# Performance work log

Hardware: AMD Instinct MI355X
Metric: run time of the kernel (lower is better)

## Reference

```python
import jax, jax.numpy as jnp
import numpy as np
from jax import lax

DIM = 192
PATCH = 8


def conv1x1(x, w):
    # x: [b,c,h,w], w: [o,c] (1x1 conv, no bias)
    return jnp.einsum('bchw,oc->bohw', x, w)


def dwconv(x, w, b, pad):
    # depthwise conv, w: [C,1,kh,kw], groups = C
    y = lax.conv_general_dilated(
        x, w, window_strides=(1, 1), padding=((pad, pad), (pad, pad)),
        dimension_numbers=('NCHW', 'OIHW', 'NCHW'),
        feature_group_count=x.shape[1])
    return y + b[None, :, None, None]


def to_patches(x, p):
    b, c, h, w = x.shape
    ph = (-h) % p
    pw = (-w) % p
    x = jnp.pad(x, ((0, 0), (0, 0), (0, ph), (0, pw)))
    H, W = h + ph, w + pw
    x = x.reshape(b, c, H // p, p, W // p, p)
    return x.transpose(0, 1, 2, 4, 3, 5)  # b c nh nw p p


def from_patches(x, h, w):
    b, c, nh, nw, p, _ = x.shape
    x = x.transpose(0, 1, 2, 4, 3, 5).reshape(b, c, nh * p, nw * p)
    return x[:, :, :h, :w]


def setup_inputs() -> dict:
    key = jax.random.key(0)
    ks = jax.random.split(key, 8)
    b, c, h, w = 4, DIM, 256, 256
    x = jax.random.normal(ks[0], (b, c, h, w), jnp.float32)
    wq = jax.random.normal(ks[1], (c, c), jnp.float32) * 0.02
    w_qdw = jax.random.normal(ks[2], (c, 1, 3, 3), jnp.float32) * 0.1
    b_qdw = jnp.zeros((c,), jnp.float32)
    wkv = jax.random.normal(ks[3], (2 * c, c), jnp.float32) * 0.02
    w_kvdw = jax.random.normal(ks[4], (2 * c, 1, 7, 7), jnp.float32) * 0.05
    b_kvdw = jnp.zeros((2 * c,), jnp.float32)
    ln_w = jnp.ones((c,), jnp.float32)
    ln_b = jnp.zeros((c,), jnp.float32)
    w_proj = jax.random.normal(ks[5], (c, c), jnp.float32) * 0.02
    b_proj = jnp.zeros((c,), jnp.float32)
    return {'x': x, 'wq': wq, 'w_qdw': w_qdw, 'b_qdw': b_qdw,
            'wkv': wkv, 'w_kvdw': w_kvdw, 'b_kvdw': b_kvdw,
            'ln_w': ln_w, 'ln_b': ln_b, 'w_proj': w_proj, 'b_proj': b_proj}


def reference(x, wq, w_qdw, b_qdw, wkv, w_kvdw, b_kvdw, ln_w, ln_b, w_proj, b_proj):
    b, c, h, w = x.shape
    p = PATCH
    q = dwconv(conv1x1(x, wq), w_qdw, b_qdw, pad=1)
    kv = dwconv(conv1x1(x, wkv), w_kvdw, b_kvdw, pad=3)
    k, v = kv[:, :c], kv[:, c:]
    qp = to_patches(q, p).astype(jnp.float32)
    kp = to_patches(k, p).astype(jnp.float32)
    out = jnp.fft.irfft2(jnp.fft.rfft2(qp) * jnp.fft.rfft2(kp), s=(p, p))
    out = from_patches(out, h, w)
    # WithBias LayerNorm over channel dim (channels-last LN in original)
    mu = out.mean(axis=1, keepdims=True)
    var = out.var(axis=1, keepdims=True)
    out = (out - mu) / jnp.sqrt(var + 1e-5)
    out = out * ln_w[None, :, None, None] + ln_b[None, :, None, None]
    out = out * v
    out = conv1x1(out, w_proj) + b_proj[None, :, None, None]
    return out
```

## Files before the change

kernel.cpp:

```cpp
#include <hip/hip_runtime.h>
#include <hip/hip_bf16.h>

#define HW 65536
#define IMG 256
static constexpr int CDIM = 192;

typedef __attribute__((ext_vector_type(8))) short short8;
typedef __attribute__((ext_vector_type(4))) float f32x4;

static __device__ __forceinline__ float b2f(unsigned short u) {
    union { unsigned u; float f; } t; t.u = ((unsigned)u) << 16; return t.f;
}
static __device__ __forceinline__ unsigned short f2bu(float f) {
    __hip_bfloat16 h = __float2bfloat16(f);
    return *reinterpret_cast<unsigned short*>(&h);
}

__global__ void pack_weights(const float* __restrict__ wq,
                             const float* __restrict__ wkv,
                             const float* __restrict__ wp,
                             __hip_bfloat16* __restrict__ Wqkv,
                             __hip_bfloat16* __restrict__ Wp) {
    int i = blockIdx.x * 256 + threadIdx.x;
    if (i < 36864) Wqkv[i] = __float2bfloat16(wq[i]);
    else if (i < 110592) Wqkv[i] = __float2bfloat16(wkv[i - 36864]);
    else if (i < 147456) Wp[i - 110592] = __float2bfloat16(wp[i - 110592]);
}

__global__ void transpose_cvt(const float* __restrict__ x,
                              __hip_bfloat16* __restrict__ xT) {
    __shared__ float tile[32][33];
    const int p0 = blockIdx.x * 32, c0 = blockIdx.y * 32;
    const int tx = threadIdx.x & 31, ty = threadIdx.x >> 5;
#pragma unroll
    for (int r = 0; r < 4; r++)
        tile[ty + r * 8][tx] = x[(size_t)(c0 + ty + r * 8) * HW + p0 + tx];
    __syncthreads();
#pragma unroll
    for (int r = 0; r < 4; r++)
        xT[(size_t)(p0 + ty + r * 8) * 192 + c0 + tx] =
            __float2bfloat16(tile[tx][ty + r * 8]);
}

__global__ void gemm_bf16(const __hip_bfloat16* __restrict__ A,
                          const __hip_bfloat16* __restrict__ Bt,
                          __hip_bfloat16* __restrict__ Y) {
    __shared__ short Bs[128][200];
    const int tid = threadIdx.x;
    const int wid = tid >> 6, lane = tid & 63;
    const int mBase = blockIdx.x * 64, nBase = blockIdx.y * 128;

#pragma unroll
    for (int l = 0; l < 12; l++) {
        int ch = tid + l * 256;
        int row = ch / 24, cc = ch % 24;
        short8 v = *(const short8*)(Bt + (size_t)(nBase + row) * 192 + cc * 8);
        *(short8*)&Bs[row][cc * 8] = v;
    }
    __syncthreads();

    const int lr = lane & 15, lg = lane >> 4;
    const __hip_bfloat16* Ab = A + (size_t)(mBase + wid * 16 + lr) * 192 + lg * 8;
    f32x4 acc[8];
#pragma unroll
    for (int f = 0; f < 8; f++) acc[f] = (f32x4){0.f, 0.f, 0.f, 0.f};

#pragma unroll
    for (int ks = 0; ks < 6; ks++) {
        short8 af = *(const short8*)(Ab + ks * 32);
#pragma unroll
        for (int f = 0; f < 8; f++) {
            short8 bfr = *(const short8*)&Bs[f * 16 + lr][ks * 32 + lg * 8];
            acc[f] = __builtin_amdgcn_mfma_f32_16x16x32_bf16(af, bfr, acc[f], 0, 0, 0);
        }
    }

    const int mrow = mBase + wid * 16 + lg * 4;
#pragma unroll
    for (int f = 0; f < 8; f++) {
        int n = nBase + f * 16 + lr;
#pragma unroll
        for (int r = 0; r < 4; r++)
            Y[(size_t)(mrow + r) * HW + n] = __float2bfloat16(acc[f][r]);
    }
}

__global__ __launch_bounds__(256) void dwconv7_v3(
    const __hip_bfloat16* __restrict__ in,
    const float* __restrict__ wdw,
    const float* __restrict__ bias,
    __hip_bfloat16* __restrict__ out) {
    __shared__ float tile[70][136];
    const int c = blockIdx.y;
    const int x0 = (blockIdx.x & 1) * 128;
    const int y0 = (blockIdx.x >> 1) * 64;
    const __hip_bfloat16* src = in + (size_t)c * HW;

    float w49[49];
#pragma unroll
    for (int i = 0; i < 49; i++) w49[i] = wdw[c * 49 + i];
    const float bval = bias[c];

#pragma unroll
    for (int l = 0; l < 5; l++) {
        int idx = threadIdx.x + l * 256;
        if (idx < 70 * 17) {
            int r = idx / 17, cs = idx - r * 17;
            int gy = y0 + r - 3;
            int gxb = x0 + cs * 8 - 3;
            if ((unsigned)gy < IMG && gxb >= 0 && gxb + 8 <= IMG) {
                short8 v = *(const short8*)(src + gy * IMG + gxb);
                f32x4 lo, hi;
#pragma unroll
                for (int e = 0; e < 4; e++) {
                    lo[e] = b2f((unsigned short)v[e]);
                    hi[e] = b2f((unsigned short)v[4 + e]);
                }
                *(f32x4*)&tile[r][cs * 8] = lo;
                *(f32x4*)&tile[r][cs * 8 + 4] = hi;
            } else {
#pragma unroll
                for (int e = 0; e < 8; e++) {
                    int gx = gxb + e;
                    float val = 0.f;
                    if ((unsigned)gy < IMG && (unsigned)gx < IMG)
                        val = b2f(*(const unsigned short*)(src + gy * IMG + gx));
                    tile[r][cs * 8 + e] = val;
                }
            }
        }
    }
    __syncthreads();

    const int tx4 = (threadIdx.x & 31) * 4;
    const int gy8 = (threadIdx.x >> 5) * 8;
    float acc[8][4];
#pragma unroll
    for (int j = 0; j < 8; j++)
#pragma unroll
        for (int xx = 0; xx < 4; xx++) acc[j][xx] = bval;

#pragma unroll
    for (int rr = 0; rr < 14; rr++) {
        f32x4 wa = *(const f32x4*)&tile[gy8 + rr][tx4];
        f32x4 wb = *(const f32x4*)&tile[gy8 + rr][tx4 + 4];
        f32x4 wc = *(const f32x4*)&tile[gy8 + rr][tx4 + 8];
        float win[12] = {wa[0], wa[1], wa[2], wa[3],
                         wb[0], wb[1], wb[2], wb[3],
                         wc[0], wc[1], wc[2], wc[3]};
#pragma unroll
        for (int j = 0; j < 8; j++) {
            const int ky = rr - j;
            if (ky >= 0 && ky < 7) {
#pragma unroll
                for (int kx = 0; kx < 7; kx++)
#pragma unroll
                    for (int xx = 0; xx < 4; xx++)
                        acc[j][xx] += win[xx + kx] * w49[ky * 7 + kx];
            }
        }
    }

    __hip_bfloat16* dst = out + (size_t)c * HW + (size_t)(y0 + gy8) * IMG + x0 + tx4;
#pragma unroll
    for (int j = 0; j < 8; j++) {
        union { unsigned short h[4]; unsigned long long u; } ob;
#pragma unroll
        for (int xx = 0; xx < 4; xx++) ob.h[xx] = f2bu(acc[j][xx]);
        *(unsigned long long*)(dst + (size_t)j * IMG) = ob.u;
    }
}

__global__ __launch_bounds__(256) void circ_qfused(
    const __hip_bfloat16* __restrict__ q0,
    const __hip_bfloat16* __restrict__ kbuf,
    const float* __restrict__ w_qdw, const float* __restrict__ b_qdw,
    __hip_bfloat16* __restrict__ sout) {
    __shared__ float qs[10][264];
    __shared__ float qP[32][68];
    __shared__ float kP[32][68];
    const int c = blockIdx.y, ph = blockIdx.x;
    const int y0 = ph * 8;
    const __hip_bfloat16* qsrc = q0 + (size_t)c * HW;
    const __hip_bfloat16* ksrc = kbuf + (size_t)c * HW;

    for (int idx = threadIdx.x; idx < 10 * 258; idx += 256) {
        int ly = idx / 258, lx = idx - ly * 258;
        int gy = y0 + ly - 1, gx = lx - 1;
        float v = 0.f;
        if ((unsigned)gy < IMG && (unsigned)gx < IMG)
            v = b2f(*(const unsigned short*)(qsrc + gy * IMG + gx));
        qs[ly][lx] = v;
    }
    {
        const int x = threadIdx.x;
#pragma unroll
        for (int a = 0; a < 8; a++) {
            float v = b2f(*(const unsigned short*)(ksrc + (y0 + a) * IMG + x));
            kP[x >> 3][a * 8 + (x & 7)] = v;
        }
    }
    __syncthreads();

    {
        const int x = threadIdx.x;
        float w9[9];
#pragma unroll
        for (int i = 0; i < 9; i++) w9[i] = w_qdw[c * 9 + i];
        float accq[8];
#pragma unroll
        for (int j = 0; j < 8; j++) accq[j] = b_qdw[c];
#pragma unroll
        for (int kx = 0; kx < 3; kx++)
#pragma unroll
            for (int yy = 0; yy < 10; yy++) {
                float vv = qs[yy][x + kx];
#pragma unroll
                for (int j = 0; j < 8; j++) {
                    int ky = yy - j;
                    if (ky >= 0 && ky < 3) accq[j] += vv * w9[ky * 3 + kx];
                }
            }
#pragma unroll
        for (int j = 0; j < 8; j++) qP[x >> 3][j * 8 + (x & 7)] = accq[j];
    }
    __syncthreads();

    const int i = threadIdx.x >> 5, pw = threadIdx.x & 31;
    float qv[8][8];
#pragma unroll
    for (int a = 0; a < 8; a++) {
        f32x4 u0 = *(const f32x4*)&qP[pw][a * 8];
        f32x4 u1 = *(const f32x4*)&qP[pw][a * 8 + 4];
        qv[a][0] = u0[0]; qv[a][1] = u0[1]; qv[a][2] = u0[2]; qv[a][3] = u0[3];
        qv[a][4] = u1[0]; qv[a][5] = u1[1]; qv[a][6] = u1[2]; qv[a][7] = u1[3];
    }
    float acc[8];
#pragma unroll
    for (int j = 0; j < 8; j++) acc[j] = 0.f;
#pragma unroll
    for (int a = 0; a < 8; a++) {
        const int r = (i - a + 8) & 7;
        f32x4 k0v = *(const f32x4*)&kP[pw][r * 8];
        f32x4 k1v = *(const f32x4*)&kP[pw][r * 8 + 4];
        float kr[8] = {k0v[0], k0v[1], k0v[2], k0v[3],
                       k1v[0], k1v[1], k1v[2], k1v[3]};
#pragma unroll
        for (int b = 0; b < 8; b++)
#pragma unroll
            for (int j = 0; j < 8; j++)
                acc[j] += qv[a][b] * kr[(j - b + 8) & 7];
    }
    union { unsigned short h[8]; short8 s8; } ob;
#pragma unroll
    for (int j = 0; j < 8; j++) ob.h[j] = f2bu(acc[j]);
    *(short8*)(sout + (size_t)c * HW + (size_t)(y0 + i) * IMG + pw * 8) = ob.s8;
}

__global__ __launch_bounds__(256, 2) void gemm_proj_ln(
    const __hip_bfloat16* __restrict__ Wp,
    const __hip_bfloat16* __restrict__ s,
    const __hip_bfloat16* __restrict__ v,
    const float* __restrict__ ln_w, const float* __restrict__ ln_b,
    const float* __restrict__ bias,
    float* __restrict__ Y) {
    __shared__ short Bs[128][200];
    __shared__ float red[2][2][128];
    __shared__ float muA[128], rsA[128];
    const int tid = threadIdx.x;
    const int p0 = blockIdx.x * 128;
    const int px = tid & 127, h = tid >> 7;
    const unsigned short* sp = (const unsigned short*)s;

    float sum = 0.f, sq = 0.f;
#pragma unroll 4
    for (int l = 0; l < 48; l++) {
        int c = h * 96 + l * 2;
        unsigned short ua = sp[(size_t)c * HW + p0 + px];
        unsigned short ub = sp[(size_t)(c + 1) * HW + p0 + px];
        float a = b2f(ua), b = b2f(ub);
        sum += a + b;
        sq += a * a + b * b;
        *(unsigned*)&Bs[px][c] = (unsigned)ua | ((unsigned)ub << 16);
    }
    red[h][0][px] = sum;
    red[h][1][px] = sq;
    __syncthreads();
    if (tid < 128) {
        float sm = red[0][0][tid] + red[1][0][tid];
        float sQ = red[0][1][tid] + red[1][1][tid];
        float mu = sm * (1.f / 192.f);
        float var = sQ * (1.f / 192.f) - mu * mu;
        muA[tid] = mu;
        rsA[tid] = rsqrtf(var + 1e-5f);
    }
    __syncthreads();

    const float mu = muA[px], rs = rsA[px];
#pragma unroll 4
    for (int l = 0; l < 48; l++) {
        int c = h * 96 + l * 2;
        unsigned pr = *(unsigned*)&Bs[px][c];
        float a = b2f((unsigned short)pr);
        float b = b2f((unsigned short)(pr >> 16));
        float va = b2f(*(const unsigned short*)(v + (size_t)c * HW + p0 + px));
        float vb = b2f(*(const unsigned short*)(v + (size_t)(c + 1) * HW + p0 + px));
        a = ((a - mu) * rs * ln_w[c] + ln_b[c]) * va;
        b = ((b - mu) * rs * ln_w[c + 1] + ln_b[c + 1]) * vb;
        *(unsigned*)&Bs[px][c] = (unsigned)f2bu(a) | ((unsigned)f2bu(b) << 16);
    }
    __syncthreads();

    const int wid = tid >> 6, lane = tid & 63;
    const int lr = lane & 15, lg = lane >> 4;
    f32x4 acc[3][8];
#pragma unroll
    for (int mf = 0; mf < 3; mf++)
#pragma unroll
        for (int f = 0; f < 8; f++) acc[mf][f] = (f32x4){0.f, 0.f, 0.f, 0.f};

#pragma unroll
    for (int ks = 0; ks < 6; ks++) {
        short8 bfr[8];
#pragma unroll
        for (int f = 0; f < 8; f++)
            bfr[f] = *(const short8*)&Bs[f * 16 + lr][ks * 32 + lg * 8];
#pragma unroll
        for (int mf = 0; mf < 3; mf++) {
            int mrow = wid * 48 + mf * 16 + lr;
            short8 af = *(const short8*)(Wp + (size_t)mrow * 192 + ks * 32 + lg * 8);
#pragma unroll
            for (int f = 0; f < 8; f++)
                acc[mf][f] = __builtin_amdgcn_mfma_f32_16x16x32_bf16(af, bfr[f], acc[mf][f], 0, 0, 0);
        }
    }

#pragma unroll
    for (int mf = 0; mf < 3; mf++) {
        int m0 = wid * 48 + mf * 16 + lg * 4;
#pragma unroll
        for (int f = 0; f < 8; f++) {
            int n = p0 + f * 16 + lr;
#pragma unroll
            for (int r = 0; r < 4; r++)
                Y[(size_t)(m0 + r) * HW + n] = acc[mf][f][r] + bias[m0 + r];
        }
    }
}

extern "C" void kernel_launch(void* const* d_in, const int* in_sizes, int n_in,
                              void* d_out, int out_size, void* d_ws, size_t ws_size,
                              hipStream_t stream) {
    const float* x      = (const float*)d_in[0];
    const float* wq     = (const float*)d_in[1];
    const float* w_qdw  = (const float*)d_in[2];
    const float* b_qdw  = (const float*)d_in[3];
    const float* wkv    = (const float*)d_in[4];
    const float* w_kvdw = (const float*)d_in[5];
    const float* b_kvdw = (const float*)d_in[6];
    const float* ln_w   = (const float*)d_in[7];
    const float* ln_b   = (const float*)d_in[8];
    const float* w_proj = (const float*)d_in[9];
    const float* b_proj = (const float*)d_in[10];
    float* out = (float*)d_out;
    char* ws = (char*)d_ws;

    __hip_bfloat16* qkv0  = (__hip_bfloat16*)(ws + 0);
    __hip_bfloat16* kvbuf = (__hip_bfloat16*)(ws + 75497472);
    __hip_bfloat16* sbuf  = (__hip_bfloat16*)(ws + 125829120);
    __hip_bfloat16* xT    = (__hip_bfloat16*)(ws + 150994944);
    __hip_bfloat16* Wqkv  = (__hip_bfloat16*)(ws + 176160768);
    __hip_bfloat16* Wp    = Wqkv + 110592;

    pack_weights<<<576, 256, 0, stream>>>(wq, wkv, w_proj, Wqkv, Wp);

    for (int b = 0; b < 4; b++) {
        const float* xb = x + (size_t)b * CDIM * HW;
        transpose_cvt<<<dim3(HW / 32, 6), 256, 0, stream>>>(xb, xT);
        gemm_bf16<<<dim3(9, HW / 128), 256, 0, stream>>>(Wqkv, xT, qkv0);
        dwconv7_v3<<<dim3(8, 384), 256, 0, stream>>>(qkv0 + (size_t)192 * HW,
                                                     w_kvdw, b_kvdw, kvbuf);
        circ_qfused<<<dim3(32, 192), 256, 0, stream>>>(qkv0, kvbuf,
                                                       w_qdw, b_qdw, sbuf);
        gemm_proj_ln<<<HW / 128, 256, 0, stream>>>(Wp, sbuf,
                                                   kvbuf + (size_t)192 * HW,
                                                   ln_w, ln_b, b_proj,
                                                   out + (size_t)b * CDIM * HW);
    }
}
```

Measured before the change: 758.2 us.

## Batch all four images into single kernel launches via blockIdx.z

Adds a batch dimension through blockIdx.z to every kernel and, when the workspace is large enough, launches each stage once over all four images instead of looping per image. This removes per-launch overhead and small-grid tails across 20 launches. In exchange it needs roughly 600 MB of workspace, and the intermediates no longer stay resident in cache between stages. A fallback keeps the per-image loop when the workspace is too small.

```diff
diff --git a/kernel.cpp b/kernel.cpp
--- a/kernel.cpp
+++ b/kernel.cpp
@@ -7,6 +7,13 @@
 
 typedef __attribute__((ext_vector_type(8))) short short8;
 typedef __attribute__((ext_vector_type(4))) float f32x4;
+
+static constexpr size_t BS_X    = (size_t)CDIM * HW;
+static constexpr size_t BS_XT   = (size_t)HW * 192;
+static constexpr size_t BS_QKV  = (size_t)576 * HW;
+static constexpr size_t BS_KV   = (size_t)384 * HW;
+static constexpr size_t BS_S    = (size_t)192 * HW;
+static constexpr size_t BS_OUT  = (size_t)192 * HW;
 
 static __device__ __forceinline__ float b2f(unsigned short u) {
     union { unsigned u; float f; } t; t.u = ((unsigned)u) << 16; return t.f;
@@ -30,6 +37,8 @@
 __global__ void transpose_cvt(const float* __restrict__ x,
                               __hip_bfloat16* __restrict__ xT) {
     __shared__ float tile[32][33];
+    x  += (size_t)blockIdx.z * BS_X;
+    xT += (size_t)blockIdx.z * BS_XT;
     const int p0 = blockIdx.x * 32, c0 = blockIdx.y * 32;
     const int tx = threadIdx.x & 31, ty = threadIdx.x >> 5;
 #pragma unroll
@@ -46,6 +55,8 @@
                           const __hip_bfloat16* __restrict__ Bt,
                           __hip_bfloat16* __restrict__ Y) {
     __shared__ short Bs[128][200];
+    Bt += (size_t)blockIdx.z * BS_XT;
+    Y  += (size_t)blockIdx.z * BS_QKV;
     const int tid = threadIdx.x;
     const int wid = tid >> 6, lane = tid & 63;
     const int mBase = blockIdx.x * 64, nBase = blockIdx.y * 128;
@@ -91,6 +102,8 @@
     const float* __restrict__ bias,
     __hip_bfloat16* __restrict__ out) {
     __shared__ float tile[70][136];
+    in  += (size_t)blockIdx.z * BS_QKV;
+    out += (size_t)blockIdx.z * BS_KV;
     const int c = blockIdx.y;
     const int x0 = (blockIdx.x & 1) * 128;
     const int y0 = (blockIdx.x >> 1) * 64;
@@ -179,6 +192,9 @@
     __shared__ float qs[10][264];
     __shared__ float qP[32][68];
     __shared__ float kP[32][68];
+    q0   += (size_t)blockIdx.z * BS_QKV;
+    kbuf += (size_t)blockIdx.z * BS_KV;
+    sout += (size_t)blockIdx.z * BS_S;
     const int c = blockIdx.y, ph = blockIdx.x;
     const int y0 = ph * 8;
     const __hip_bfloat16* qsrc = q0 + (size_t)c * HW;
@@ -267,6 +283,9 @@
     __shared__ short Bs[128][200];
     __shared__ float red[2][2][128];
     __shared__ float muA[128], rsA[128];
+    s += (size_t)blockIdx.z * BS_S;
+    v += (size_t)blockIdx.z * BS_KV;
+    Y += (size_t)blockIdx.z * BS_OUT;
     const int tid = threadIdx.x;
     const int p0 = blockIdx.x * 128;
     const int px = tid & 127, h = tid >> 7;
@@ -365,26 +384,46 @@
     float* out = (float*)d_out;
     char* ws = (char*)d_ws;
 
-    __hip_bfloat16* qkv0  = (__hip_bfloat16*)(ws + 0);
-    __hip_bfloat16* kvbuf = (__hip_bfloat16*)(ws + 75497472);
-    __hip_bfloat16* sbuf  = (__hip_bfloat16*)(ws + 125829120);
-    __hip_bfloat16* xT    = (__hip_bfloat16*)(ws + 150994944);
-    __hip_bfloat16* Wqkv  = (__hip_bfloat16*)(ws + 176160768);
-    __hip_bfloat16* Wp    = Wqkv + 110592;
-
-    pack_weights<<<576, 256, 0, stream>>>(wq, wkv, w_proj, Wqkv, Wp);
-
-    for (int b = 0; b < 4; b++) {
-        const float* xb = x + (size_t)b * CDIM * HW;
-        transpose_cvt<<<dim3(HW / 32, 6), 256, 0, stream>>>(xb, xT);
-        gemm_bf16<<<dim3(9, HW / 128), 256, 0, stream>>>(Wqkv, xT, qkv0);
-        dwconv7_v3<<<dim3(8, 384), 256, 0, stream>>>(qkv0 + (size_t)192 * HW,
-                                                     w_kvdw, b_kvdw, kvbuf);
-        circ_qfused<<<dim3(32, 192), 256, 0, stream>>>(qkv0, kvbuf,
-                                                       w_qdw, b_qdw, sbuf);
-        gemm_proj_ln<<<HW / 128, 256, 0, stream>>>(Wp, sbuf,
-                                                   kvbuf + (size_t)192 * HW,
-                                                   ln_w, ln_b, b_proj,
-                                                   out + (size_t)b * CDIM * HW);
-    }
-}
+    const size_t BATCHED_NEED = 604200960ull;
+    const bool batched = (ws_size >= BATCHED_NEED);
+
+    if (batched) {
+        __hip_bfloat16* qkv0  = (__hip_bfloat16*)(ws + 0);
+        __hip_bfloat16* kvbuf = (__hip_bfloat16*)(ws + 301989888ull);
+        __hip_bfloat16* xT    = (__hip_bfloat16*)(ws + 503316480ull);
+        __hip_bfloat16* sbuf  = xT;
+        __hip_bfloat16* Wqkv  = (__hip_bfloat16*)(ws + 603979776ull);
+        __hip_bfloat16* Wp    = Wqkv + 110592;
+
+        pack_weights<<<576, 256, 0, stream>>>(wq, wkv, w_proj, Wqkv, Wp);
+        transpose_cvt<<<dim3(HW / 32, 6, 4), 256, 0, stream>>>(x, xT);
+        gemm_bf16<<<dim3(9, HW / 128, 4), 256, 0, stream>>>(Wqkv, xT, qkv0);
+        dwconv7_v3<<<dim3(8, 384, 4), 256, 0, stream>>>(qkv0 + (size_t)192 * HW,
+                                                        w_kvdw, b_kvdw, kvbuf);
+        circ_qfused<<<dim3(32, 192, 4), 256, 0, stream>>>(qkv0, kvbuf,
+                                                          w_qdw, b_qdw, sbuf);
+        gemm_proj_ln<<<dim3(HW / 128, 1, 4), 256, 0, stream>>>(
+            Wp, sbuf, kvbuf + (size_t)192 * HW, ln_w, ln_b, b_proj, out);
+    } else {
+        __hip_bfloat16* qkv0  = (__hip_bfloat16*)(ws + 0);
+        __hip_bfloat16* kvbuf = (__hip_bfloat16*)(ws + 75497472ull);
+        __hip_bfloat16* sbuf  = (__hip_bfloat16*)(ws + 125829120ull);
+        __hip_bfloat16* xT    = (__hip_bfloat16*)(ws + 150994944ull);
+        __hip_bfloat16* Wqkv  = (__hip_bfloat16*)(ws + 176160768ull);
+        __hip_bfloat16* Wp    = Wqkv + 110592;
+
+        pack_weights<<<576, 256, 0, stream>>>(wq, wkv, w_proj, Wqkv, Wp);
+        for (int b = 0; b < 4; b++) {
+            const float* xb = x + (size_t)b * BS_X;
+            transpose_cvt<<<dim3(HW / 32, 6, 1), 256, 0, stream>>>(xb, xT);
+            gemm_bf16<<<dim3(9, HW / 128, 1), 256, 0, stream>>>(Wqkv, xT, qkv0);
+            dwconv7_v3<<<dim3(8, 384, 1), 256, 0, stream>>>(qkv0 + (size_t)192 * HW,
+                                                            w_kvdw, b_kvdw, kvbuf);
+            circ_qfused<<<dim3(32, 192, 1), 256, 0, stream>>>(qkv0, kvbuf,
+                                                              w_qdw, b_qdw, sbuf);
+            gemm_proj_ln<<<dim3(HW / 128, 1, 1), 256, 0, stream>>>(
+                Wp, sbuf, kvbuf + (size_t)192 * HW, ln_w, ln_b, b_proj,
+                out + (size_t)b * BS_OUT);
+        }
+    }
+}
```

After: 815.6 us. 1.08x slower.
